# Kernel optimization log

Hardware: AMD Instinct MI355X
Metric: run time of the kernel (lower is better)

## Reference

```python
import jax, jax.numpy as jnp
import numpy as np

B, LQ, LK = 8, 1024, 1024
Q_IN, K_IN, D = 256, 256, 512
H = 8
DK = D // H


def _linear_params(key, in_dim, out_dim):
    k1, k2 = jax.random.split(key)
    bound = 1.0 / np.sqrt(in_dim)
    W = jax.random.uniform(k1, (in_dim, out_dim), jnp.float32, -bound, bound)
    b = jax.random.uniform(k2, (out_dim,), jnp.float32, -bound, bound)
    return W, b


def setup_inputs() -> dict:
    key = jax.random.key(0)
    ks = jax.random.split(key, 7)
    query = jax.random.normal(ks[0], (B, LQ, Q_IN), jnp.float32)
    kv = jax.random.normal(ks[1], (B, LK, K_IN), jnp.float32)
    mask = jax.random.randint(ks[2], (B, LQ, LK), 0, 2, jnp.int32)
    Wq, bq = _linear_params(ks[3], Q_IN, D)
    Wk, bk = _linear_params(ks[4], K_IN, D)
    Wv, bv = _linear_params(ks[5], K_IN, D)
    Wo, bo = _linear_params(ks[6], D, D)
    return {"query": query, "key": kv, "mask": mask,
            "Wq": Wq, "bq": bq, "Wk": Wk, "bk": bk,
            "Wv": Wv, "bv": bv, "Wo": Wo, "bo": bo}


def reference(query, key, mask, Wq, bq, Wk, bk, Wv, bv, Wo, bo):
    b = query.shape[0]
    # ReLU-activated QKV projections
    q = jax.nn.relu(query @ Wq + bq)   # [B, Lq, D]
    v = jax.nn.relu(key @ Wv + bv)     # [B, Lk, D]
    k = jax.nn.relu(key @ Wk + bk)     # [B, Lk, D]
    # split heads: [B, H, L, d_k]
    q = q.reshape(b, -1, H, DK).transpose(0, 2, 1, 3)
    k = k.reshape(b, -1, H, DK).transpose(0, 2, 1, 3)
    v = v.reshape(b, -1, H, DK).transpose(0, 2, 1, 3)
    scores = jnp.einsum('bhqd,bhkd->bhqk', q, k) / jnp.sqrt(jnp.float32(DK))
    scores = jnp.where(mask[:, None, :, :] == 0, jnp.float32(-1e8), scores)
    attn = jax.nn.softmax(scores, axis=-1)
    out = jnp.einsum('bhqk,bhkd->bhqd', attn, v)
    out = out.transpose(0, 2, 1, 3).reshape(b, -1, D)
    return out @ Wo + bo
```

## Files before the change

### kernel.cpp

```cpp
#include <hip/hip_runtime.h>
#include <hip/hip_bf16.h>
#include <type_traits>

typedef __bf16 bf16_t;
typedef __bf16 bf16x4 __attribute__((ext_vector_type(4)));
typedef __bf16 bf16x8 __attribute__((ext_vector_type(8)));
typedef float  f32x4  __attribute__((ext_vector_type(4)));

__device__ __forceinline__ f32x4 mfma16(bf16x8 a, bf16x8 b, f32x4 c) {
  return __builtin_amdgcn_mfma_f32_16x16x32_bf16(a, b, c, 0, 0, 0);
}

static constexpr int NB = 8;
static constexpr int LQ = 1024;
static constexpr int LKk = 1024;
static constexpr int DMODEL = 512;
static constexpr int NH = 8;
static constexpr int DKH = 64;
static constexpr int MROWS = NB * LQ;
static constexpr int MWORDS = NB * LQ * (LKk / 64);
#define KSCALE 0.1803368801111204f

__device__ __forceinline__ int swz(int row, int byte) {
  return row * 128 + (byte ^ ((row & 7) << 4));
}

__global__ __launch_bounds__(256)
void mask_pack(const int* __restrict__ mask, unsigned long long* __restrict__ mpk) {
  const int wd = blockIdx.x * 256 + threadIdx.x;
  const int4* base = reinterpret_cast<const int4*>(mask + (size_t)wd * 64);
  unsigned long long bits = 0;
  #pragma unroll
  for (int i = 0; i < 16; ++i) {
    int4 v = base[i];
    bits |= (unsigned long long)(v.x != 0) << (4 * i);
    bits |= (unsigned long long)(v.y != 0) << (4 * i + 1);
    bits |= (unsigned long long)(v.z != 0) << (4 * i + 2);
    bits |= (unsigned long long)(v.w != 0) << (4 * i + 3);
  }
  mpk[wd] = bits;
}

__device__ __forceinline__ void wt_tile(const float* __restrict__ W, bf16_t* __restrict__ Wt,
                                        int K, int N, int kt, int nt, int t) {
  __shared__ bf16_t T[64][72];
  const int k0 = kt * 64, n0 = nt * 64;
  const int kr = t >> 2, c0 = (t & 3) * 16;
  const float4* src = reinterpret_cast<const float4*>(W + (size_t)(k0 + kr) * N + n0 + c0);
  #pragma unroll
  for (int j = 0; j < 4; ++j) {
    float4 f = src[j];
    T[c0 + j * 4 + 0][kr] = (bf16_t)f.x;
    T[c0 + j * 4 + 1][kr] = (bf16_t)f.y;
    T[c0 + j * 4 + 2][kr] = (bf16_t)f.z;
    T[c0 + j * 4 + 3][kr] = (bf16_t)f.w;
  }
  __syncthreads();
  const int nr = t >> 2, kc0 = (t & 3) * 16;
  bf16_t* dst = Wt + (size_t)(n0 + nr) * K + k0 + kc0;
  #pragma unroll
  for (int j = 0; j < 2; ++j)
    *reinterpret_cast<bf16x8*>(dst + j * 8) =
        *reinterpret_cast<const bf16x8*>(&T[nr][kc0 + j * 8]);
}

__global__ __launch_bounds__(256)
void weight_prep(const float* __restrict__ Wq, const float* __restrict__ Wk,
                 const float* __restrict__ Wv, const float* __restrict__ Wo,
                 bf16_t* __restrict__ Wtq, bf16_t* __restrict__ Wtk,
                 bf16_t* __restrict__ Wtv, bf16_t* __restrict__ Wto) {
  const int bidx = blockIdx.x, t = threadIdx.x;
  if (bidx < 32)        wt_tile(Wq, Wtq, 256, 512, bidx >> 3, bidx & 7, t);
  else if (bidx < 64)   wt_tile(Wk, Wtk, 256, 512, (bidx - 32) >> 3, bidx & 7, t);
  else if (bidx < 96)   wt_tile(Wv, Wtv, 256, 512, (bidx - 64) >> 3, bidx & 7, t);
  else                  wt_tile(Wo, Wto, 512, 512, (bidx - 96) >> 3, bidx & 7, t);
}

template<int K, bool RELU, typename AT, typename OT>
__global__ __launch_bounds__(256)
void gemm_bias_act(const AT* __restrict__ A, const bf16_t* __restrict__ Wt,
                   const float* __restrict__ bias, OT* __restrict__ C,
                   float postscale)
{
  constexpr int N = 512;
  __shared__ alignas(16) char Alds[64 * 128];
  __shared__ alignas(16) char Wlds[64 * 128];
  const int t = threadIdx.x;
  const int l = t & 63, w = t >> 6;
  const int xcd = blockIdx.x & 7, idx = blockIdx.x >> 3;
  const int m0 = (xcd * 16 + (idx >> 3)) * 64, n0 = (idx & 7) * 64;

  f32x4 acc[4] = {};
  for (int k0 = 0; k0 < K; k0 += 64) {
    __syncthreads();
    if constexpr (std::is_same<AT, float>::value) {
      const int row = t >> 2, c0 = (t & 3) * 16;
      const float4* ap = reinterpret_cast<const float4*>(A + (size_t)(m0 + row) * K + k0 + c0);
      #pragma unroll
      for (int j = 0; j < 4; ++j) {
        float4 f = ap[j];
        bf16x4 o = { (bf16_t)f.x, (bf16_t)f.y, (bf16_t)f.z, (bf16_t)f.w };
        *reinterpret_cast<bf16x4*>(&Alds[swz(row, (c0 + j * 4) * 2)]) = o;
      }
    } else {
      const int row = t >> 2, cb = ((2 * t) & 7) * 16;
      const bf16_t* src = A + (size_t)(m0 + row) * K + k0 + cb / 2;
      *reinterpret_cast<bf16x8*>(&Alds[swz(row, cb)]) = *reinterpret_cast<const bf16x8*>(src);
      *reinterpret_cast<bf16x8*>(&Alds[swz(row, cb + 16)]) = *reinterpret_cast<const bf16x8*>(src + 8);
    }
    {
      const int row = t >> 2, cb = ((2 * t) & 7) * 16;
      const bf16_t* src = Wt + (size_t)(n0 + row) * K + k0 + cb / 2;
      *reinterpret_cast<bf16x8*>(&Wlds[swz(row, cb)]) = *reinterpret_cast<const bf16x8*>(src);
      *reinterpret_cast<bf16x8*>(&Wlds[swz(row, cb + 16)]) = *reinterpret_cast<const bf16x8*>(src + 8);
    }
    __syncthreads();
    #pragma unroll
    for (int ks = 0; ks < 2; ++ks) {
      const int kb = (ks * 32 + ((l >> 4) * 8)) * 2;
      const int arow = w * 16 + (l & 15);
      bf16x8 af = *reinterpret_cast<const bf16x8*>(&Alds[swz(arow, kb)]);
      #pragma unroll
      for (int ct = 0; ct < 4; ++ct) {
        const int brow = ct * 16 + (l & 15);
        bf16x8 bfr = *reinterpret_cast<const bf16x8*>(&Wlds[swz(brow, kb)]);
        acc[ct] = mfma16(af, bfr, acc[ct]);
      }
    }
  }
  #pragma unroll
  for (int ct = 0; ct < 4; ++ct) {
    const int col = n0 + ct * 16 + (l & 15);
    const float bv = bias[col];
    #pragma unroll
    for (int r = 0; r < 4; ++r) {
      const int row = m0 + w * 16 + ((l >> 4) * 4) + r;
      float x = acc[ct][r] + bv;
      if constexpr (RELU) x = fmaxf(x, 0.f);
      C[(size_t)row * N + col] = (OT)(x * postscale);
    }
  }
}

__global__ __launch_bounds__(256)
void gemm_kv(const float* __restrict__ A, const bf16_t* __restrict__ Wtk,
             const bf16_t* __restrict__ Wtv, const float* __restrict__ bk,
             const float* __restrict__ bv, bf16_t* __restrict__ Ck,
             bf16_t* __restrict__ Vt)
{
  constexpr int K = 256, N = 512;
  __shared__ alignas(16) char Alds[64 * 128];
  __shared__ alignas(16) char Wk_lds[64 * 128];
  __shared__ alignas(16) char Wv_lds[64 * 128];
  const int t = threadIdx.x;
  const int l = t & 63, w = t >> 6;
  const int xcd = blockIdx.x & 7, idx = blockIdx.x >> 3;
  const int m0 = (xcd * 16 + (idx >> 3)) * 64, n0 = (idx & 7) * 64;

  f32x4 acck[4] = {}, accv[4] = {};
  for (int k0 = 0; k0 < K; k0 += 64) {
    __syncthreads();
    {
      const int row = t >> 2, c0 = (t & 3) * 16;
      const float4* ap = reinterpret_cast<const float4*>(A + (size_t)(m0 + row) * K + k0 + c0);
      #pragma unroll
      for (int j = 0; j < 4; ++j) {
        float4 f = ap[j];
        bf16x4 o = { (bf16_t)f.x, (bf16_t)f.y, (bf16_t)f.z, (bf16_t)f.w };
        *reinterpret_cast<bf16x4*>(&Alds[swz(row, (c0 + j * 4) * 2)]) = o;
      }
    }
    {
      const int row = t >> 2, cb = ((2 * t) & 7) * 16;
      const bf16_t* sk = Wtk + (size_t)(n0 + row) * K + k0 + cb / 2;
      const bf16_t* sv = Wtv + (size_t)(n0 + row) * K + k0 + cb / 2;
      *reinterpret_cast<bf16x8*>(&Wk_lds[swz(row, cb)]) = *reinterpret_cast<const bf16x8*>(sk);
      *reinterpret_cast<bf16x8*>(&Wk_lds[swz(row, cb + 16)]) = *reinterpret_cast<const bf16x8*>(sk + 8);
      *reinterpret_cast<bf16x8*>(&Wv_lds[swz(row, cb)]) = *reinterpret_cast<const bf16x8*>(sv);
      *reinterpret_cast<bf16x8*>(&Wv_lds[swz(row, cb + 16)]) = *reinterpret_cast<const bf16x8*>(sv + 8);
    }
    __syncthreads();
    #pragma unroll
    for (int ks = 0; ks < 2; ++ks) {
      const int kb = (ks * 32 + ((l >> 4) * 8)) * 2;
      const int arow = w * 16 + (l & 15);
      bf16x8 af = *reinterpret_cast<const bf16x8*>(&Alds[swz(arow, kb)]);
      #pragma unroll
      for (int ct = 0; ct < 4; ++ct) {
        const int brow = ct * 16 + (l & 15);
        bf16x8 bk8 = *reinterpret_cast<const bf16x8*>(&Wk_lds[swz(brow, kb)]);
        bf16x8 bv8 = *reinterpret_cast<const bf16x8*>(&Wv_lds[swz(brow, kb)]);
        acck[ct] = mfma16(af, bk8, acck[ct]);
        accv[ct] = mfma16(af, bv8, accv[ct]);
      }
    }
  }
  const int row0 = m0 + w * 16 + ((l >> 4) * 4);
  const int vb = row0 >> 10;
  const int kv = row0 & 1023;
  #pragma unroll
  for (int ct = 0; ct < 4; ++ct) {
    const int col = n0 + ct * 16 + (l & 15);
    const float bkv = bk[col], bvv = bv[col];
    #pragma unroll
    for (int r = 0; r < 4; ++r)
      Ck[(size_t)(row0 + r) * N + col] = (bf16_t)(fmaxf(acck[ct][r] + bkv, 0.f) * KSCALE);
    bf16x4 vv;
    #pragma unroll
    for (int r = 0; r < 4; ++r) vv[r] = (bf16_t)fmaxf(accv[ct][r] + bvv, 0.f);
    bf16_t* dst = Vt + (((size_t)vb * NH + (col >> 6)) * DKH + (col & 63)) * LKk + kv;
    *reinterpret_cast<bf16x4*>(dst) = vv;
  }
}

__global__ __launch_bounds__(256)
void attn_kernel(const bf16_t* __restrict__ Qp, const bf16_t* __restrict__ Kp,
                 const bf16_t* __restrict__ Vt, const unsigned long long* __restrict__ Mpk,
                 bf16_t* __restrict__ AO)
{
  __shared__ alignas(16) char Klds[64 * 128];
  __shared__ alignas(16) char Vlds[64 * 128];
  __shared__ alignas(16) char Plds[4 * 32 * 128];
  const int t = threadIdx.x, l = t & 63, w = t >> 6;
  const int g = l >> 4, qh = l & 15;
  const int bid = (blockIdx.x & 7) * 64 + (blockIdx.x >> 3);
  const int qt = bid & 7, h = (bid >> 3) & 7, b = bid >> 6;
  const int wq0 = qt * 128 + w * 32;
  const size_t rb = (size_t)b * LQ;
  const bf16_t* vtb = Vt + ((size_t)b * NH + h) * DKH * LKk;

  bf16x8 qf[2][2];
  #pragma unroll
  for (int j = 0; j < 2; ++j)
    #pragma unroll
    for (int ks = 0; ks < 2; ++ks)
      qf[j][ks] = *reinterpret_cast<const bf16x8*>(
          Qp + (rb + wq0 + j * 16 + qh) * DMODEL + h * DKH + ks * 32 + g * 8);

  const unsigned long long* mrow0 = Mpk + (rb + wq0 + qh) * (LKk / 64);
  const unsigned long long* mrow1 = Mpk + (rb + wq0 + 16 + qh) * (LKk / 64);

  f32x4 acc[2][4] = {};
  float mrun[2] = { -1e30f, -1e30f }, lsum[2] = { 0.f, 0.f };

  for (int kv0 = 0; kv0 < LKk; kv0 += 64) {
    const unsigned long long mw[2] = { mrow0[kv0 >> 6], mrow1[kv0 >> 6] };

    __syncthreads();
    {
      const int row = t >> 2, cb = ((2 * t) & 7) * 16;
      const bf16_t* src = Kp + (rb + kv0 + row) * DMODEL + h * DKH + cb / 2;
      *reinterpret_cast<bf16x8*>(&Klds[swz(row, cb)]) = *reinterpret_cast<const bf16x8*>(src);
      *reinterpret_cast<bf16x8*>(&Klds[swz(row, cb + 16)]) = *reinterpret_cast<const bf16x8*>(src + 8);
    }
    {
      const int row = t >> 2, cb = ((2 * t) & 7) * 16;
      const bf16_t* src = vtb + (size_t)row * LKk + kv0 + cb / 2;
      *reinterpret_cast<bf16x8*>(&Vlds[swz(row, cb)]) = *reinterpret_cast<const bf16x8*>(src);
      *reinterpret_cast<bf16x8*>(&Vlds[swz(row, cb + 16)]) = *reinterpret_cast<const bf16x8*>(src + 8);
    }
    __syncthreads();

    f32x4 s[2][4] = {};
    #pragma unroll
    for (int ks = 0; ks < 2; ++ks) {
      const int kb = (ks * 32 + g * 8) * 2;
      #pragma unroll
      for (int ct = 0; ct < 4; ++ct) {
        bf16x8 kf = *reinterpret_cast<const bf16x8*>(&Klds[swz(ct * 16 + qh, kb)]);
        s[0][ct] = mfma16(kf, qf[0][ks], s[0][ct]);
        s[1][ct] = mfma16(kf, qf[1][ks], s[1][ct]);
      }
    }

    #pragma unroll
    for (int j = 0; j < 2; ++j) {
      float rmax = -1e30f;
      #pragma unroll
      for (int ct = 0; ct < 4; ++ct) {
        #pragma unroll
        for (int r = 0; r < 4; ++r) {
          float x = ((mw[j] >> (ct * 16 + g * 4 + r)) & 1) ? s[j][ct][r] : -1e8f;
          s[j][ct][r] = x;
          rmax = fmaxf(rmax, x);
        }
      }
      rmax = fmaxf(rmax, __shfl_xor(rmax, 16));
      rmax = fmaxf(rmax, __shfl_xor(rmax, 32));
      const float newm = fmaxf(mrun[j], rmax);

      if (__any(newm > mrun[j])) {
        const float scale = __builtin_amdgcn_exp2f(mrun[j] - newm);
        lsum[j] *= scale;
        #pragma unroll
        for (int r = 0; r < 4; ++r) {
          const float sr = __shfl(scale, g * 4 + r, 64);
          #pragma unroll
          for (int dct = 0; dct < 4; ++dct) acc[j][dct][r] *= sr;
        }
        mrun[j] = newm;
      }

      float psum = 0.f;
      #pragma unroll
      for (int ct = 0; ct < 4; ++ct) {
        #pragma unroll
        for (int r = 0; r < 4; ++r) {
          const float pv = __builtin_amdgcn_exp2f(s[j][ct][r] - mrun[j]);
          s[j][ct][r] = pv;
          psum += pv;
        }
      }
      psum += __shfl_xor(psum, 16);
      psum += __shfl_xor(psum, 32);
      lsum[j] += psum;

      #pragma unroll
      for (int ct = 0; ct < 4; ++ct) {
        #pragma unroll
        for (int r = 0; r < 4; ++r)
          *reinterpret_cast<bf16_t*>(
              &Plds[w * 4096 + swz(j * 16 + qh, (ct * 16 + g * 4 + r) * 2)]) =
              (bf16_t)s[j][ct][r];
      }
    }

    #pragma unroll
    for (int ks = 0; ks < 2; ++ks) {
      const int kb = (ks * 32 + g * 8) * 2;
      bf16x8 pf0 = *reinterpret_cast<const bf16x8*>(&Plds[w * 4096 + swz(qh, kb)]);
      bf16x8 pf1 = *reinterpret_cast<const bf16x8*>(&Plds[w * 4096 + swz(16 + qh, kb)]);
      #pragma unroll
      for (int dct = 0; dct < 4; ++dct) {
        bf16x8 vf = *reinterpret_cast<const bf16x8*>(&Vlds[swz(dct * 16 + qh, kb)]);
        acc[0][dct] = mfma16(pf0, vf, acc[0][dct]);
        acc[1][dct] = mfma16(pf1, vf, acc[1][dct]);
      }
    }
  }

  #pragma unroll
  for (int j = 0; j < 2; ++j) {
    const float inv = 1.0f / lsum[j];
    float invr[4];
    #pragma unroll
    for (int r = 0; r < 4; ++r) invr[r] = __shfl(inv, g * 4 + r, 64);
    #pragma unroll
    for (int dct = 0; dct < 4; ++dct) {
      const int col = h * DKH + dct * 16 + qh;
      #pragma unroll
      for (int r = 0; r < 4; ++r) {
        const int q = wq0 + j * 16 + g * 4 + r;
        AO[(rb + q) * DMODEL + col] = (bf16_t)(acc[j][dct][r] * invr[r]);
      }
    }
  }
}

extern "C" void kernel_launch(void* const* d_in, const int* in_sizes, int n_in,
                              void* d_out, int out_size, void* d_ws, size_t ws_size,
                              hipStream_t stream)
{
  const float* query = (const float*)d_in[0];
  const float* keyin = (const float*)d_in[1];
  const int*   mask  = (const int*)d_in[2];
  const float* Wq = (const float*)d_in[3];
  const float* bq = (const float*)d_in[4];
  const float* Wk = (const float*)d_in[5];
  const float* bk = (const float*)d_in[6];
  const float* Wv = (const float*)d_in[7];
  const float* bv = (const float*)d_in[8];
  const float* Wo = (const float*)d_in[9];
  const float* bo = (const float*)d_in[10];
  float* out = (float*)d_out;

  bf16_t* Qp = (bf16_t*)d_ws;
  bf16_t* Kp = Qp + (size_t)MROWS * DMODEL;
  bf16_t* Vt = Kp + (size_t)MROWS * DMODEL;
  bf16_t* AO = Vt + (size_t)MROWS * DMODEL;
  unsigned long long* Mpk = (unsigned long long*)(AO + (size_t)MROWS * DMODEL);
  bf16_t* Wtq = (bf16_t*)(Mpk + MWORDS);
  bf16_t* Wtk = Wtq + 512 * 256;
  bf16_t* Wtv = Wtk + 512 * 256;
  bf16_t* Wto = Wtv + 512 * 256;

  dim3 blk(256);

  weight_prep<<<dim3(160), blk, 0, stream>>>(Wq, Wk, Wv, Wo, Wtq, Wtk, Wtv, Wto);
  mask_pack<<<dim3(MWORDS / 256), blk, 0, stream>>>(mask, Mpk);
  gemm_bias_act<256, true, float, bf16_t><<<dim3(1024), blk, 0, stream>>>(query, Wtq, bq, Qp, 1.0f);
  gemm_kv<<<dim3(1024), blk, 0, stream>>>(keyin, Wtk, Wtv, bk, bv, Kp, Vt);

  attn_kernel<<<dim3(NB * NH * (LQ / 128)), blk, 0, stream>>>(Qp, Kp, Vt, Mpk, AO);

  gemm_bias_act<512, false, bf16_t, float><<<dim3(1024), blk, 0, stream>>>(AO, Wto, bo, out, 1.0f);
}
```

Before: 97.43 us.

## Split attention KV range across two blocks and fuse combine into output GEMM

Attention work is split along the key dimension into two halves, doubling the block count from 512 to 1024 so more of the GPU is occupied. Each half writes unnormalized fp32 partial outputs plus running max and sum. The output projection GEMM merges the two partials with flash-decoding style rescaling while staging its A tile. This costs two fp32 partial buffers of about 16 MB each in extra global traffic, plus a second online-softmax pass. It runs only when the workspace is large enough, otherwise it falls back to the original path.

Measured after the change: 116.6 us. 19.6% more time.

```diff
diff --git a/kernel.cpp b/kernel.cpp
--- a/kernel.cpp
+++ b/kernel.cpp
@@ -213,18 +213,15 @@
   }
 }
 
-__global__ __launch_bounds__(256)
-void attn_kernel(const bf16_t* __restrict__ Qp, const bf16_t* __restrict__ Kp,
-                 const bf16_t* __restrict__ Vt, const unsigned long long* __restrict__ Mpk,
-                 bf16_t* __restrict__ AO)
-{
-  __shared__ alignas(16) char Klds[64 * 128];
-  __shared__ alignas(16) char Vlds[64 * 128];
-  __shared__ alignas(16) char Plds[4 * 32 * 128];
+template<bool SPLIT>
+__device__ __forceinline__ void attn_core(
+    const bf16_t* __restrict__ Qp, const bf16_t* __restrict__ Kp,
+    const bf16_t* __restrict__ Vt, const unsigned long long* __restrict__ Mpk,
+    bf16_t* __restrict__ AO, float* __restrict__ Od, float* __restrict__ ml,
+    int b, int h, int qt, int kvbeg, int kvend, char* Plds)
+{
   const int t = threadIdx.x, l = t & 63, w = t >> 6;
   const int g = l >> 4, qh = l & 15;
-  const int bid = (blockIdx.x & 7) * 64 + (blockIdx.x >> 3);
-  const int qt = bid & 7, h = (bid >> 3) & 7, b = bid >> 6;
   const int wq0 = qt * 128 + w * 32;
   const size_t rb = (size_t)b * LQ;
   const bf16_t* vtb = Vt + ((size_t)b * NH + h) * DKH * LKk;
@@ -243,21 +240,21 @@
   f32x4 acc[2][4] = {};
   float mrun[2] = { -1e30f, -1e30f }, lsum[2] = { 0.f, 0.f };
 
-  for (int kv0 = 0; kv0 < LKk; kv0 += 64) {
+  for (int kv0 = kvbeg; kv0 < kvend; kv0 += 64) {
     const unsigned long long mw[2] = { mrow0[kv0 >> 6], mrow1[kv0 >> 6] };
 
     __syncthreads();
     {
       const int row = t >> 2, cb = ((2 * t) & 7) * 16;
       const bf16_t* src = Kp + (rb + kv0 + row) * DMODEL + h * DKH + cb / 2;
-      *reinterpret_cast<bf16x8*>(&Klds[swz(row, cb)]) = *reinterpret_cast<const bf16x8*>(src);
-      *reinterpret_cast<bf16x8*>(&Klds[swz(row, cb + 16)]) = *reinterpret_cast<const bf16x8*>(src + 8);
+      *reinterpret_cast<bf16x8*>(&Plds[-16384 + swz(row, cb)]) = *reinterpret_cast<const bf16x8*>(src);
+      *reinterpret_cast<bf16x8*>(&Plds[-16384 + swz(row, cb + 16)]) = *reinterpret_cast<const bf16x8*>(src + 8);
     }
     {
       const int row = t >> 2, cb = ((2 * t) & 7) * 16;
       const bf16_t* src = vtb + (size_t)row * LKk + kv0 + cb / 2;
-      *reinterpret_cast<bf16x8*>(&Vlds[swz(row, cb)]) = *reinterpret_cast<const bf16x8*>(src);
-      *reinterpret_cast<bf16x8*>(&Vlds[swz(row, cb + 16)]) = *reinterpret_cast<const bf16x8*>(src + 8);
+      *reinterpret_cast<bf16x8*>(&Plds[-8192 + swz(row, cb)]) = *reinterpret_cast<const bf16x8*>(src);
+      *reinterpret_cast<bf16x8*>(&Plds[-8192 + swz(row, cb + 16)]) = *reinterpret_cast<const bf16x8*>(src + 8);
     }
     __syncthreads();
 
@@ -267,7 +264,7 @@
       const int kb = (ks * 32 + g * 8) * 2;
       #pragma unroll
       for (int ct = 0; ct < 4; ++ct) {
-        bf16x8 kf = *reinterpret_cast<const bf16x8*>(&Klds[swz(ct * 16 + qh, kb)]);
+        bf16x8 kf = *reinterpret_cast<const bf16x8*>(&Plds[-16384 + swz(ct * 16 + qh, kb)]);
         s[0][ct] = mfma16(kf, qf[0][ks], s[0][ct]);
         s[1][ct] = mfma16(kf, qf[1][ks], s[1][ct]);
       }
@@ -332,27 +329,148 @@
       bf16x8 pf1 = *reinterpret_cast<const bf16x8*>(&Plds[w * 4096 + swz(16 + qh, kb)]);
       #pragma unroll
       for (int dct = 0; dct < 4; ++dct) {
-        bf16x8 vf = *reinterpret_cast<const bf16x8*>(&Vlds[swz(dct * 16 + qh, kb)]);
+        bf16x8 vf = *reinterpret_cast<const bf16x8*>(&Plds[-8192 + swz(dct * 16 + qh, kb)]);
         acc[0][dct] = mfma16(pf0, vf, acc[0][dct]);
         acc[1][dct] = mfma16(pf1, vf, acc[1][dct]);
       }
     }
   }
 
-  #pragma unroll
-  for (int j = 0; j < 2; ++j) {
-    const float inv = 1.0f / lsum[j];
-    float invr[4];
-    #pragma unroll
-    for (int r = 0; r < 4; ++r) invr[r] = __shfl(inv, g * 4 + r, 64);
-    #pragma unroll
-    for (int dct = 0; dct < 4; ++dct) {
-      const int col = h * DKH + dct * 16 + qh;
-      #pragma unroll
-      for (int r = 0; r < 4; ++r) {
-        const int q = wq0 + j * 16 + g * 4 + r;
-        AO[(rb + q) * DMODEL + col] = (bf16_t)(acc[j][dct][r] * invr[r]);
-      }
+  if constexpr (SPLIT) {
+    #pragma unroll
+    for (int j = 0; j < 2; ++j) {
+      #pragma unroll
+      for (int dct = 0; dct < 4; ++dct) {
+        const int col = h * DKH + dct * 16 + qh;
+        #pragma unroll
+        for (int r = 0; r < 4; ++r) {
+          const int q = wq0 + j * 16 + g * 4 + r;
+          Od[(rb + q) * DMODEL + col] = acc[j][dct][r];
+        }
+      }
+      if (g == 0) {
+        const size_t mi = ((rb + wq0 + j * 16 + qh) * NH + h) * 2;
+        ml[mi]     = mrun[j];
+        ml[mi + 1] = lsum[j];
+      }
+    }
+  } else {
+    #pragma unroll
+    for (int j = 0; j < 2; ++j) {
+      const float inv = 1.0f / lsum[j];
+      float invr[4];
+      #pragma unroll
+      for (int r = 0; r < 4; ++r) invr[r] = __shfl(inv, g * 4 + r, 64);
+      #pragma unroll
+      for (int dct = 0; dct < 4; ++dct) {
+        const int col = h * DKH + dct * 16 + qh;
+        #pragma unroll
+        for (int r = 0; r < 4; ++r) {
+          const int q = wq0 + j * 16 + g * 4 + r;
+          AO[(rb + q) * DMODEL + col] = (bf16_t)(acc[j][dct][r] * invr[r]);
+        }
+      }
+    }
+  }
+}
+
+__global__ __launch_bounds__(256)
+void attn_kernel(const bf16_t* __restrict__ Qp, const bf16_t* __restrict__ Kp,
+                 const bf16_t* __restrict__ Vt, const unsigned long long* __restrict__ Mpk,
+                 bf16_t* __restrict__ AO)
+{
+  __shared__ alignas(16) char SM[32768];
+  const int bid = (blockIdx.x & 7) * 64 + (blockIdx.x >> 3);
+  const int qt = bid & 7, h = (bid >> 3) & 7, b = bid >> 6;
+  attn_core<false>(Qp, Kp, Vt, Mpk, AO, nullptr, nullptr,
+                   b, h, qt, 0, LKk, SM + 16384);
+}
+
+__global__ __launch_bounds__(256)
+void attn_split(const bf16_t* __restrict__ Qp, const bf16_t* __restrict__ Kp,
+                const bf16_t* __restrict__ Vt, const unsigned long long* __restrict__ Mpk,
+                float* __restrict__ O0, float* __restrict__ O1,
+                float* __restrict__ ml0, float* __restrict__ ml1)
+{
+  __shared__ alignas(16) char SM[32768];
+  const int raw = blockIdx.x;
+  const int bid = (raw & 7) * 128 + (raw >> 3);
+  const int hw = bid & 1;
+  const int bid2 = bid >> 1;
+  const int qt = bid2 & 7, h = (bid2 >> 3) & 7, b = bid2 >> 6;
+  attn_core<true>(Qp, Kp, Vt, Mpk, nullptr,
+                  hw ? O1 : O0, hw ? ml1 : ml0,
+                  b, h, qt, hw * 512, hw * 512 + 512, SM + 16384);
+}
+
+__global__ __launch_bounds__(256)
+void gemm_out_combine(const float* __restrict__ O0, const float* __restrict__ O1,
+                      const float* __restrict__ ml0, const float* __restrict__ ml1,
+                      const bf16_t* __restrict__ Wt, const float* __restrict__ bias,
+                      float* __restrict__ C)
+{
+  constexpr int K = 512, N = 512;
+  __shared__ alignas(16) char Alds[64 * 128];
+  __shared__ alignas(16) char Wlds[64 * 128];
+  const int t = threadIdx.x;
+  const int l = t & 63, w = t >> 6;
+  const int xcd = blockIdx.x & 7, idx = blockIdx.x >> 3;
+  const int m0 = (xcd * 16 + (idx >> 3)) * 64, n0 = (idx & 7) * 64;
+  const int arow_g = m0 + (t >> 2);
+
+  f32x4 acc[4] = {};
+  for (int k0 = 0; k0 < K; k0 += 64) {
+    const int hd = k0 >> 6;
+    const size_t mi = ((size_t)arow_g * NH + hd) * 2;
+    const float m0v = ml0[mi], l0v = ml0[mi + 1];
+    const float m1v = ml1[mi], l1v = ml1[mi + 1];
+    const float M = fmaxf(m0v, m1v);
+    float w0 = __builtin_amdgcn_exp2f(m0v - M);
+    float w1 = __builtin_amdgcn_exp2f(m1v - M);
+    const float inv = 1.0f / (l0v * w0 + l1v * w1);
+    w0 *= inv; w1 *= inv;
+
+    __syncthreads();
+    {
+      const int row = t >> 2, c0 = (t & 3) * 16;
+      const float4* a0 = reinterpret_cast<const float4*>(O0 + (size_t)(m0 + row) * K + k0 + c0);
+      const float4* a1 = reinterpret_cast<const float4*>(O1 + (size_t)(m0 + row) * K + k0 + c0);
+      #pragma unroll
+      for (int j = 0; j < 4; ++j) {
+        float4 fa = a0[j], fb = a1[j];
+        bf16x4 o = { (bf16_t)(fa.x * w0 + fb.x * w1), (bf16_t)(fa.y * w0 + fb.y * w1),
+                     (bf16_t)(fa.z * w0 + fb.z * w1), (bf16_t)(fa.w * w0 + fb.w * w1) };
+        *reinterpret_cast<bf16x4*>(&Alds[swz(row, (c0 + j * 4) * 2)]) = o;
+      }
+    }
+    {
+      const int row = t >> 2, cb = ((2 * t) & 7) * 16;
+      const bf16_t* src = Wt + (size_t)(n0 + row) * K + k0 + cb / 2;
+      *reinterpret_cast<bf16x8*>(&Wlds[swz(row, cb)]) = *reinterpret_cast<const bf16x8*>(src);
+      *reinterpret_cast<bf16x8*>(&Wlds[swz(row, cb + 16)]) = *reinterpret_cast<const bf16x8*>(src + 8);
+    }
+    __syncthreads();
+    #pragma unroll
+    for (int ks = 0; ks < 2; ++ks) {
+      const int kb = (ks * 32 + ((l >> 4) * 8)) * 2;
+      const int arow = w * 16 + (l & 15);
+      bf16x8 af = *reinterpret_cast<const bf16x8*>(&Alds[swz(arow, kb)]);
+      #pragma unroll
+      for (int ct = 0; ct < 4; ++ct) {
+        const int brow = ct * 16 + (l & 15);
+        bf16x8 bfr = *reinterpret_cast<const bf16x8*>(&Wlds[swz(brow, kb)]);
+        acc[ct] = mfma16(af, bfr, acc[ct]);
+      }
+    }
+  }
+  #pragma unroll
+  for (int ct = 0; ct < 4; ++ct) {
+    const int col = n0 + ct * 16 + (l & 15);
+    const float bv = bias[col];
+    #pragma unroll
+    for (int r = 0; r < 4; ++r) {
+      const int row = m0 + w * 16 + ((l >> 4) * 4) + r;
+      C[(size_t)row * N + col] = acc[ct][r] + bv;
     }
   }
 }
@@ -383,6 +501,12 @@
   bf16_t* Wtk = Wtq + 512 * 256;
   bf16_t* Wtv = Wtk + 512 * 256;
   bf16_t* Wto = Wtv + 512 * 256;
+  float*  O0  = (float*)(Wto + 512 * 512);
+  float*  O1  = O0 + (size_t)MROWS * DMODEL;
+  float*  ml0 = O1 + (size_t)MROWS * DMODEL;
+  float*  ml1 = ml0 + (size_t)MROWS * NH * 2;
+  const size_t need = (size_t)((char*)(ml1 + (size_t)MROWS * NH * 2) - (char*)d_ws);
+  const bool split = ws_size >= need;
 
   dim3 blk(256);
 
@@ -391,7 +515,11 @@
   gemm_bias_act<256, true, float, bf16_t><<<dim3(1024), blk, 0, stream>>>(query, Wtq, bq, Qp, 1.0f);
   gemm_kv<<<dim3(1024), blk, 0, stream>>>(keyin, Wtk, Wtv, bk, bv, Kp, Vt);
 
-  attn_kernel<<<dim3(NB * NH * (LQ / 128)), blk, 0, stream>>>(Qp, Kp, Vt, Mpk, AO);
-
-  gemm_bias_act<512, false, bf16_t, float><<<dim3(1024), blk, 0, stream>>>(AO, Wto, bo, out, 1.0f);
-}
+  if (split) {
+    attn_split<<<dim3(1024), blk, 0, stream>>>(Qp, Kp, Vt, Mpk, O0, O1, ml0, ml1);
+    gemm_out_combine<<<dim3(1024), blk, 0, stream>>>(O0, O1, ml0, ml1, Wto, bo, out);
+  } else {
+    attn_kernel<<<dim3(NB * NH * (LQ / 128)), blk, 0, stream>>>(Qp, Kp, Vt, Mpk, AO);
+    gemm_bias_act<512, false, bf16_t, float><<<dim3(1024), blk, 0, stream>>>(AO, Wto, bo, out, 1.0f);
+  }
+}
```

## Double attention query tile per block to 256 rows, 64 per wave

Applied to the files above, without the earlier changes.

Each attention block now covers 256 query rows, with each wave owning 64 rows (4 MFMA row groups instead of 2). Every K/V tile staged in LDS is therefore reused across twice as many queries, which halves global K/V traffic and the number of barriers per unit of work. The P tile is also written to LDS as packed bf16x4 stores instead of scalar stores. In exchange the grid halves to 256 blocks, register pressure rises (acc and s arrays double), and LDS grows to 48KB, which may reduce occupancy and CU fill.

After: 106.2 us. 9.0% more time.

```diff
diff --git a/kernel.cpp b/kernel.cpp
--- a/kernel.cpp
+++ b/kernel.cpp
@@ -218,33 +218,37 @@
                  const bf16_t* __restrict__ Vt, const unsigned long long* __restrict__ Mpk,
                  bf16_t* __restrict__ AO)
 {
-  __shared__ alignas(16) char Klds[64 * 128];
-  __shared__ alignas(16) char Vlds[64 * 128];
-  __shared__ alignas(16) char Plds[4 * 32 * 128];
+  __shared__ alignas(16) char SM[49152];
+  char* Klds = SM;
+  char* Vlds = SM + 8192;
   const int t = threadIdx.x, l = t & 63, w = t >> 6;
   const int g = l >> 4, qh = l & 15;
-  const int bid = (blockIdx.x & 7) * 64 + (blockIdx.x >> 3);
-  const int qt = bid & 7, h = (bid >> 3) & 7, b = bid >> 6;
-  const int wq0 = qt * 128 + w * 32;
+  char* Pw = SM + 16384 + w * 8192;
+  const int bid = (blockIdx.x & 7) * 32 + (blockIdx.x >> 3);
+  const int qt = bid & 3, h = (bid >> 2) & 7, b = bid >> 5;
+  const int wq0 = qt * 256 + w * 64;
   const size_t rb = (size_t)b * LQ;
   const bf16_t* vtb = Vt + ((size_t)b * NH + h) * DKH * LKk;
 
-  bf16x8 qf[2][2];
-  #pragma unroll
-  for (int j = 0; j < 2; ++j)
+  bf16x8 qf[4][2];
+  #pragma unroll
+  for (int j = 0; j < 4; ++j)
     #pragma unroll
     for (int ks = 0; ks < 2; ++ks)
       qf[j][ks] = *reinterpret_cast<const bf16x8*>(
           Qp + (rb + wq0 + j * 16 + qh) * DMODEL + h * DKH + ks * 32 + g * 8);
 
-  const unsigned long long* mrow0 = Mpk + (rb + wq0 + qh) * (LKk / 64);
-  const unsigned long long* mrow1 = Mpk + (rb + wq0 + 16 + qh) * (LKk / 64);
-
-  f32x4 acc[2][4] = {};
-  float mrun[2] = { -1e30f, -1e30f }, lsum[2] = { 0.f, 0.f };
+  const unsigned long long* mrow = Mpk + (rb + wq0 + qh) * (LKk / 64);
+
+  f32x4 acc[4][4] = {};
+  float mrun[4] = { -1e30f, -1e30f, -1e30f, -1e30f };
+  float lsum[4] = {};
 
   for (int kv0 = 0; kv0 < LKk; kv0 += 64) {
-    const unsigned long long mw[2] = { mrow0[kv0 >> 6], mrow1[kv0 >> 6] };
+    unsigned long long mw[4];
+    #pragma unroll
+    for (int j = 0; j < 4; ++j)
+      mw[j] = mrow[(size_t)(j * 16) * (LKk / 64) + (kv0 >> 6)];
 
     __syncthreads();
     {
@@ -261,20 +265,21 @@
     }
     __syncthreads();
 
-    f32x4 s[2][4] = {};
+    f32x4 s[4][4] = {};
     #pragma unroll
     for (int ks = 0; ks < 2; ++ks) {
       const int kb = (ks * 32 + g * 8) * 2;
       #pragma unroll
       for (int ct = 0; ct < 4; ++ct) {
         bf16x8 kf = *reinterpret_cast<const bf16x8*>(&Klds[swz(ct * 16 + qh, kb)]);
-        s[0][ct] = mfma16(kf, qf[0][ks], s[0][ct]);
-        s[1][ct] = mfma16(kf, qf[1][ks], s[1][ct]);
-      }
-    }
-
-    #pragma unroll
-    for (int j = 0; j < 2; ++j) {
+        #pragma unroll
+        for (int j = 0; j < 4; ++j)
+          s[j][ct] = mfma16(kf, qf[j][ks], s[j][ct]);
+      }
+    }
+
+    #pragma unroll
+    for (int j = 0; j < 4; ++j) {
       float rmax = -1e30f;
       #pragma unroll
       for (int ct = 0; ct < 4; ++ct) {
@@ -317,30 +322,31 @@
 
       #pragma unroll
       for (int ct = 0; ct < 4; ++ct) {
-        #pragma unroll
-        for (int r = 0; r < 4; ++r)
-          *reinterpret_cast<bf16_t*>(
-              &Plds[w * 4096 + swz(j * 16 + qh, (ct * 16 + g * 4 + r) * 2)]) =
-              (bf16_t)s[j][ct][r];
+        bf16x4 pk = { (bf16_t)s[j][ct][0], (bf16_t)s[j][ct][1],
+                      (bf16_t)s[j][ct][2], (bf16_t)s[j][ct][3] };
+        *reinterpret_cast<bf16x4*>(&Pw[swz(j * 16 + qh, (ct * 16 + g * 4) * 2)]) = pk;
       }
     }
 
     #pragma unroll
     for (int ks = 0; ks < 2; ++ks) {
       const int kb = (ks * 32 + g * 8) * 2;
-      bf16x8 pf0 = *reinterpret_cast<const bf16x8*>(&Plds[w * 4096 + swz(qh, kb)]);
-      bf16x8 pf1 = *reinterpret_cast<const bf16x8*>(&Plds[w * 4096 + swz(16 + qh, kb)]);
+      bf16x8 pf[4];
+      #pragma unroll
+      for (int j = 0; j < 4; ++j)
+        pf[j] = *reinterpret_cast<const bf16x8*>(&Pw[swz(j * 16 + qh, kb)]);
       #pragma unroll
       for (int dct = 0; dct < 4; ++dct) {
         bf16x8 vf = *reinterpret_cast<const bf16x8*>(&Vlds[swz(dct * 16 + qh, kb)]);
-        acc[0][dct] = mfma16(pf0, vf, acc[0][dct]);
-        acc[1][dct] = mfma16(pf1, vf, acc[1][dct]);
-      }
-    }
-  }
-
-  #pragma unroll
-  for (int j = 0; j < 2; ++j) {
+        #pragma unroll
+        for (int j = 0; j < 4; ++j)
+          acc[j][dct] = mfma16(pf[j], vf, acc[j][dct]);
+      }
+    }
+  }
+
+  #pragma unroll
+  for (int j = 0; j < 4; ++j) {
     const float inv = 1.0f / lsum[j];
     float invr[4];
     #pragma unroll
@@ -391,7 +397,7 @@
   gemm_bias_act<256, true, float, bf16_t><<<dim3(1024), blk, 0, stream>>>(query, Wtq, bq, Qp, 1.0f);
   gemm_kv<<<dim3(1024), blk, 0, stream>>>(keyin, Wtk, Wtv, bk, bv, Kp, Vt);
 
-  attn_kernel<<<dim3(NB * NH * (LQ / 128)), blk, 0, stream>>>(Qp, Kp, Vt, Mpk, AO);
+  attn_kernel<<<dim3(NB * NH * (LQ / 256)), blk, 0, stream>>>(Qp, Kp, Vt, Mpk, AO);
 
   gemm_bias_act<512, false, bf16_t, float><<<dim3(1024), blk, 0, stream>>>(AO, Wto, bo, out, 1.0f);
 }
```
